# Kernel optimization log

Measured on AMD Instinct MI355X. Metric: run time of the kernel, lower is better.

Reference implementation:

```python
import jax, jax.numpy as jnp
import numpy as np


def setup_inputs() -> dict:
    key = jax.random.key(0)
    ks = jax.random.split(key, 8)
    B, S, D, H = 32, 8192, 256, 256  # batch, seq_len, input_dim, hidden_dim
    bound = 1.0 / np.sqrt(H)
    x = jax.random.normal(ks[0], (B, H), dtype=jnp.float32)
    context = jax.random.normal(ks[1], (B, S, D), dtype=jnp.float32)
    mask = jax.random.randint(ks[2], (B, S), 0, 2, dtype=jnp.int32)
    # input_linear: Linear(H, H)
    W_in = jax.random.uniform(ks[3], (H, H), jnp.float32, -bound, bound)
    b_in = jax.random.uniform(ks[4], (H,), jnp.float32, -bound, bound)
    # context_linear: Conv1d(D, H, kernel=1) == pointwise linear over features
    W_ctx = jax.random.uniform(ks[5], (H, D), jnp.float32, -1.0 / np.sqrt(D), 1.0 / np.sqrt(D))
    b_ctx = jax.random.uniform(ks[6], (H,), jnp.float32, -1.0 / np.sqrt(D), 1.0 / np.sqrt(D))
    V = jax.random.uniform(ks[7], (H,), jnp.float32, -bound, bound)
    return {"x": x, "context": context, "mask": mask,
            "W_in": W_in, "b_in": b_in, "W_ctx": W_ctx, "b_ctx": b_ctx, "V": V}


def reference(x, context, mask, W_in, b_in, W_ctx, b_ctx, V):
    # inp: [B, H] -> broadcast over seq as [B, 1, H]
    inp = (x @ W_in.T + b_in)[:, None, :]
    # ctx: Conv1d(kernel=1) over permuted context == per-position linear: [B, S, H]
    ctx = jnp.einsum('bsd,hd->bsh', context, W_ctx) + b_ctx
    # score: V . tanh(inp + ctx) reduced over H -> [B, S]
    att = jnp.einsum('bsh,h->bs', jnp.tanh(inp + ctx), V)
    att = 10.0 * jnp.tanh(att)
    att = jnp.where(mask.astype(bool), att, -jnp.inf)
    ans = jax.nn.softmax(att, axis=1)
    indices = jnp.argmax(ans, axis=1)
    p = jnp.max(ans, axis=1)
    return (indices, p[:, None], mask.astype(bool))
```

## Files before the change

### kernel.cpp

```cpp
#include <hip/hip_runtime.h>
#include <math.h>

#define S_LEN 8192
#define BATCH 32
#define HDIM 256
#define DDIM 256
#define TS 32
#define LDK 264

typedef float f32x4 __attribute__((ext_vector_type(4)));
typedef __fp16 h16x2 __attribute__((ext_vector_type(2)));
typedef __fp16 h16x4 __attribute__((ext_vector_type(4)));
typedef _Float16 f16x4 __attribute__((ext_vector_type(4)));
typedef _Float16 f16x8 __attribute__((ext_vector_type(8)));

static __device__ __forceinline__ float fast_tanh(float x) {
    float e = __expf(2.0f * x);
    return 1.0f - 2.0f / (e + 1.0f);
}

__global__ void prep_kernel(const float* __restrict__ x,
                            const float* __restrict__ W_in,
                            const float* __restrict__ b_in,
                            const float* __restrict__ W_ctx,
                            const float* __restrict__ b_ctx,
                            float* __restrict__ cin,
                            _Float16* __restrict__ Wf) {
    __shared__ float xs[DDIM];
    const int bx = blockIdx.x;
    const int t  = threadIdx.x;
    if (bx < BATCH) {
        xs[t] = x[bx * DDIM + t];
        __syncthreads();
        const float* wr = W_in + t * DDIM;
        float acc = b_in[t] + b_ctx[t];
        #pragma unroll 8
        for (int d = 0; d < DDIM; ++d) acc += xs[d] * wr[d];
        cin[bx * HDIM + t] = acc;
    } else {
        const int g  = (bx - BATCH) * 256 + t;
        const int nt = g >> 9;
        const int ks = (g >> 6) & 7;
        const int l  = g & 63;
        const int h  = nt * 16 + (l & 15);
        const int d0 = ks * 32 + (l >> 4) * 8;
        const float* src = W_ctx + h * DDIM + d0;
        f16x8 vh;
        #pragma unroll
        for (int j = 0; j < 8; ++j) vh[j] = (_Float16)src[j];
        *(f16x8*)(Wf + (size_t)g * 8) = vh;
    }
}

__launch_bounds__(256, 4)
__global__ void att_kernel(const float* __restrict__ context,
                           const int* __restrict__ mask,
                           const float* __restrict__ cin,
                           const float* __restrict__ V,
                           const _Float16* __restrict__ Wf,
                           float* __restrict__ att,
                           float* __restrict__ out_mask) {
    __shared__ _Float16 a_hi[TS * LDK];
    __shared__ _Float16 a_lo[TS * LDK];
    __shared__ float cin_s[HDIM];
    __shared__ float v_s[HDIM];
    __shared__ float att_part[4][TS];

    const int sblk = blockIdx.x;
    const int b    = blockIdx.y;
    const int t    = threadIdx.x;
    const int w    = t >> 6;
    const int l    = t & 63;
    const int lane16 = l & 15;
    const int q      = l >> 4;

    cin_s[t] = cin[b * HDIM + t];
    v_s[t]   = V[t];

    const float* cbase = context + ((size_t)b * S_LEN + (size_t)sblk * TS) * DDIM;
    #pragma unroll
    for (int i = 0; i < 8; ++i) {
        int f   = i * 256 + t;
        int row = f >> 6;
        int c4  = f & 63;
        f32x4 v = *(const f32x4*)(cbase + row * DDIM + c4 * 4);
        h16x2 h0 = __builtin_amdgcn_cvt_pkrtz(v[0], v[1]);
        h16x2 h1 = __builtin_amdgcn_cvt_pkrtz(v[2], v[3]);
        h16x2 l0 = __builtin_amdgcn_cvt_pkrtz(v[0] - (float)h0[0], v[1] - (float)h0[1]);
        h16x2 l1 = __builtin_amdgcn_cvt_pkrtz(v[2] - (float)h1[0], v[3] - (float)h1[1]);
        h16x4 hi; hi[0] = h0[0]; hi[1] = h0[1]; hi[2] = h1[0]; hi[3] = h1[1];
        h16x4 lo; lo[0] = l0[0]; lo[1] = l0[1]; lo[2] = l1[0]; lo[3] = l1[1];
        *(h16x4*)(a_hi + row * LDK + c4 * 4) = hi;
        *(h16x4*)(a_lo + row * LDK + c4 * 4) = lo;
    }
    __syncthreads();

    f32x4 acc[2][4];
    #pragma unroll
    for (int mt = 0; mt < 2; ++mt)
        #pragma unroll
        for (int i = 0; i < 4; ++i) acc[mt][i] = (f32x4){0.f, 0.f, 0.f, 0.f};

    const int ntb = w * 4;
    #pragma unroll
    for (int ks = 0; ks < 8; ++ks) {
        f16x8 bh[4];
        #pragma unroll
        for (int i = 0; i < 4; ++i) {
            int off = (((ntb + i) * 8 + ks) * 64 + l) * 8;
            bh[i] = *(const f16x8*)(Wf + off);
        }
        f16x8 ah[2], al[2];
        #pragma unroll
        for (int mt = 0; mt < 2; ++mt) {
            int o = (mt * 16 + lane16) * LDK + ks * 32 + q * 8;
            ah[mt] = *(const f16x8*)(a_hi + o);
            al[mt] = *(const f16x8*)(a_lo + o);
        }
        #pragma unroll
        for (int mt = 0; mt < 2; ++mt)
            #pragma unroll
            for (int i = 0; i < 4; ++i) {
                acc[mt][i] = __builtin_amdgcn_mfma_f32_16x16x32_f16(ah[mt], bh[i], acc[mt][i], 0, 0, 0);
                acc[mt][i] = __builtin_amdgcn_mfma_f32_16x16x32_f16(al[mt], bh[i], acc[mt][i], 0, 0, 0);
            }
    }

    float part[2][4] = {};
    #pragma unroll
    for (int i = 0; i < 4; ++i) {
        int h = (ntb + i) * 16 + lane16;
        float c  = cin_s[h];
        float vv = v_s[h];
        #pragma unroll
        for (int mt = 0; mt < 2; ++mt)
            #pragma unroll
            for (int r = 0; r < 4; ++r)
                part[mt][r] += fast_tanh(acc[mt][i][r] + c) * vv;
    }
    #pragma unroll
    for (int mt = 0; mt < 2; ++mt)
        #pragma unroll
        for (int r = 0; r < 4; ++r) {
            float v = part[mt][r];
            v += __shfl_xor(v, 1);
            v += __shfl_xor(v, 2);
            v += __shfl_xor(v, 4);
            v += __shfl_xor(v, 8);
            part[mt][r] = v;
        }
    if (lane16 == 0) {
        #pragma unroll
        for (int mt = 0; mt < 2; ++mt)
            #pragma unroll
            for (int r = 0; r < 4; ++r)
                att_part[w][mt * 16 + q * 4 + r] = part[mt][r];
    }
    __syncthreads();

    if (t < TS) {
        float a = att_part[0][t] + att_part[1][t] + att_part[2][t] + att_part[3][t];
        a = 10.0f * fast_tanh(a);
        int s  = sblk * TS + t;
        int mk = mask[b * S_LEN + s];
        att[(size_t)b * S_LEN + s] = mk ? a : -INFINITY;
        out_mask[(size_t)b * S_LEN + s] = mk ? 1.0f : 0.0f;
    }
}

__global__ void reduce_kernel(const float* __restrict__ att,
                              float* __restrict__ out) {
    __shared__ float smax[256];
    __shared__ int   sidx[256];
    const int b = blockIdx.x;
    const int t = threadIdx.x;
    const float* row = att + (size_t)b * S_LEN;

    float best = -INFINITY;
    int   bid  = 0x7fffffff;
    for (int s = t; s < S_LEN; s += 256) {
        float v = row[s];
        if (v > best) { best = v; bid = s; }
    }
    smax[t] = best; sidx[t] = bid;
    __syncthreads();
    for (int off = 128; off > 0; off >>= 1) {
        if (t < off) {
            float ov = smax[t + off]; int oi = sidx[t + off];
            if (ov > smax[t] || (ov == smax[t] && oi < sidx[t])) { smax[t] = ov; sidx[t] = oi; }
        }
        __syncthreads();
    }
    const float mx = smax[0];
    const int   ix = sidx[0];
    __syncthreads();

    float sum = 0.f;
    for (int s = t; s < S_LEN; s += 256)
        sum += __expf(row[s] - mx);
    smax[t] = sum;
    __syncthreads();
    for (int off = 128; off > 0; off >>= 1) {
        if (t < off) smax[t] += smax[t + off];
        __syncthreads();
    }
    if (t == 0) {
        out[b]         = (float)ix;
        out[BATCH + b] = 1.0f / smax[0];
    }
}

extern "C" void kernel_launch(void* const* d_in, const int* in_sizes, int n_in,
                              void* d_out, int out_size, void* d_ws, size_t ws_size,
                              hipStream_t stream) {
    const float* x       = (const float*)d_in[0];
    const float* context = (const float*)d_in[1];
    const int*   mask    = (const int*)d_in[2];
    const float* W_in    = (const float*)d_in[3];
    const float* b_in    = (const float*)d_in[4];
    const float* W_ctx   = (const float*)d_in[5];
    const float* b_ctx   = (const float*)d_in[6];
    const float* V       = (const float*)d_in[7];
    float* out = (float*)d_out;

    char* ws = (char*)d_ws;
    float*    cin = (float*)ws;
    _Float16* Wf  = (_Float16*)(ws + 32 * 1024);
    float*    att = (float*)(ws + 160 * 1024);

    float* out_mask = out + 64;

    prep_kernel<<<64, 256, 0, stream>>>(x, W_in, b_in, W_ctx, b_ctx, cin, Wf);
    dim3 grid(S_LEN / TS, BATCH);
    att_kernel<<<grid, 256, 0, stream>>>(context, mask, cin, V, Wf, att, out_mask);
    reduce_kernel<<<BATCH, 256, 0, stream>>>(att, out);
}
```

Before: 434.6 us.

## Persistent 1024-thread blocks with register-resident W and double-buffered context tiles

Each block now handles 512 sequence positions in 8 sub-tiles of 64, using 16 waves. Each wave keeps its 16-row slice of the fp16 W_ctx in registers and swaps the MFMA operand roles. The next context sub-tile is prefetched into registers and converted into a second LDS buffer while the current one is computed. This removes repeated global W loads per block and overlaps context loads with MFMA work. In exchange the grid is much smaller (512 blocks of 1024 threads), which raises register pressure and lowers occupancy.

```diff
diff --git a/kernel.cpp b/kernel.cpp
--- a/kernel.cpp
+++ b/kernel.cpp
@@ -5,18 +5,30 @@
 #define BATCH 32
 #define HDIM 256
 #define DDIM 256
-#define TS 32
+#define SCHUNK 512
+#define NSUB 8
+#define TSUB 64
 #define LDK 264
 
 typedef float f32x4 __attribute__((ext_vector_type(4)));
 typedef __fp16 h16x2 __attribute__((ext_vector_type(2)));
 typedef __fp16 h16x4 __attribute__((ext_vector_type(4)));
-typedef _Float16 f16x4 __attribute__((ext_vector_type(4)));
 typedef _Float16 f16x8 __attribute__((ext_vector_type(8)));
 
 static __device__ __forceinline__ float fast_tanh(float x) {
     float e = __expf(2.0f * x);
     return 1.0f - 2.0f / (e + 1.0f);
+}
+
+static __device__ __forceinline__ void cvt_store(f32x4 v, _Float16* ph, _Float16* pl) {
+    h16x2 h0 = __builtin_amdgcn_cvt_pkrtz(v[0], v[1]);
+    h16x2 h1 = __builtin_amdgcn_cvt_pkrtz(v[2], v[3]);
+    h16x2 l0 = __builtin_amdgcn_cvt_pkrtz(v[0] - (float)h0[0], v[1] - (float)h0[1]);
+    h16x2 l1 = __builtin_amdgcn_cvt_pkrtz(v[2] - (float)h1[0], v[3] - (float)h1[1]);
+    h16x4 hi; hi[0] = h0[0]; hi[1] = h0[1]; hi[2] = h1[0]; hi[3] = h1[1];
+    h16x4 lo; lo[0] = l0[0]; lo[1] = l0[1]; lo[2] = l1[0]; lo[3] = l1[1];
+    *(h16x4*)ph = hi;
+    *(h16x4*)pl = lo;
 }
 
 __global__ void prep_kernel(const float* __restrict__ x,
@@ -39,10 +51,10 @@
         cin[bx * HDIM + t] = acc;
     } else {
         const int g  = (bx - BATCH) * 256 + t;
-        const int nt = g >> 9;
+        const int ht = g >> 9;
         const int ks = (g >> 6) & 7;
         const int l  = g & 63;
-        const int h  = nt * 16 + (l & 15);
+        const int h  = ht * 16 + (l & 15);
         const int d0 = ks * 32 + (l >> 4) * 8;
         const float* src = W_ctx + h * DDIM + d0;
         f16x8 vh;
@@ -52,7 +64,7 @@
     }
 }
 
-__launch_bounds__(256, 4)
+__launch_bounds__(1024, 4)
 __global__ void att_kernel(const float* __restrict__ context,
                            const int* __restrict__ mask,
                            const float* __restrict__ cin,
@@ -60,111 +72,101 @@
                            const _Float16* __restrict__ Wf,
                            float* __restrict__ att,
                            float* __restrict__ out_mask) {
-    __shared__ _Float16 a_hi[TS * LDK];
-    __shared__ _Float16 a_lo[TS * LDK];
-    __shared__ float cin_s[HDIM];
-    __shared__ float v_s[HDIM];
-    __shared__ float att_part[4][TS];
-
-    const int sblk = blockIdx.x;
-    const int b    = blockIdx.y;
-    const int t    = threadIdx.x;
-    const int w    = t >> 6;
-    const int l    = t & 63;
+    __shared__ __align__(16) _Float16 a_hi[2][TSUB * LDK];
+    __shared__ __align__(16) _Float16 a_lo[2][TSUB * LDK];
+    __shared__ float att_part[2][16][TSUB];
+
+    const int schunk = blockIdx.x;
+    const int b      = blockIdx.y;
+    const int t      = threadIdx.x;
+    const int w      = t >> 6;
+    const int l      = t & 63;
     const int lane16 = l & 15;
     const int q      = l >> 4;
 
-    cin_s[t] = cin[b * HDIM + t];
-    v_s[t]   = V[t];
-
-    const float* cbase = context + ((size_t)b * S_LEN + (size_t)sblk * TS) * DDIM;
+    f16x8 wfrag[8];
     #pragma unroll
-    for (int i = 0; i < 8; ++i) {
-        int f   = i * 256 + t;
-        int row = f >> 6;
-        int c4  = f & 63;
-        f32x4 v = *(const f32x4*)(cbase + row * DDIM + c4 * 4);
-        h16x2 h0 = __builtin_amdgcn_cvt_pkrtz(v[0], v[1]);
-        h16x2 h1 = __builtin_amdgcn_cvt_pkrtz(v[2], v[3]);
-        h16x2 l0 = __builtin_amdgcn_cvt_pkrtz(v[0] - (float)h0[0], v[1] - (float)h0[1]);
-        h16x2 l1 = __builtin_amdgcn_cvt_pkrtz(v[2] - (float)h1[0], v[3] - (float)h1[1]);
-        h16x4 hi; hi[0] = h0[0]; hi[1] = h0[1]; hi[2] = h1[0]; hi[3] = h1[1];
-        h16x4 lo; lo[0] = l0[0]; lo[1] = l0[1]; lo[2] = l1[0]; lo[3] = l1[1];
-        *(h16x4*)(a_hi + row * LDK + c4 * 4) = hi;
-        *(h16x4*)(a_lo + row * LDK + c4 * 4) = lo;
-    }
-    __syncthreads();
-
-    f32x4 acc[2][4];
+    for (int ks = 0; ks < 8; ++ks)
+        wfrag[ks] = *(const f16x8*)(Wf + (size_t)((w * 8 + ks) * 64 + l) * 8);
+
+    float cinr[4], vr[4];
     #pragma unroll
-    for (int mt = 0; mt < 2; ++mt)
-        #pragma unroll
-        for (int i = 0; i < 4; ++i) acc[mt][i] = (f32x4){0.f, 0.f, 0.f, 0.f};
-
-    const int ntb = w * 4;
-    #pragma unroll
-    for (int ks = 0; ks < 8; ++ks) {
-        f16x8 bh[4];
-        #pragma unroll
-        for (int i = 0; i < 4; ++i) {
-            int off = (((ntb + i) * 8 + ks) * 64 + l) * 8;
-            bh[i] = *(const f16x8*)(Wf + off);
-        }
-        f16x8 ah[2], al[2];
-        #pragma unroll
-        for (int mt = 0; mt < 2; ++mt) {
-            int o = (mt * 16 + lane16) * LDK + ks * 32 + q * 8;
-            ah[mt] = *(const f16x8*)(a_hi + o);
-            al[mt] = *(const f16x8*)(a_lo + o);
-        }
-        #pragma unroll
-        for (int mt = 0; mt < 2; ++mt)
-            #pragma unroll
-            for (int i = 0; i < 4; ++i) {
-                acc[mt][i] = __builtin_amdgcn_mfma_f32_16x16x32_f16(ah[mt], bh[i], acc[mt][i], 0, 0, 0);
-                acc[mt][i] = __builtin_amdgcn_mfma_f32_16x16x32_f16(al[mt], bh[i], acc[mt][i], 0, 0, 0);
-            }
-    }
-
-    float part[2][4] = {};
+    for (int r = 0; r < 4; ++r) {
+        int h = w * 16 + q * 4 + r;
+        cinr[r] = cin[b * HDIM + h];
+        vr[r]   = V[h];
+    }
+
+    const float* cbase = context + ((size_t)b * S_LEN + (size_t)schunk * SCHUNK) * DDIM;
+
     #pragma unroll
     for (int i = 0; i < 4; ++i) {
-        int h = (ntb + i) * 16 + lane16;
-        float c  = cin_s[h];
-        float vv = v_s[h];
-        #pragma unroll
-        for (int mt = 0; mt < 2; ++mt)
+        int f = i * 1024 + t, row = f >> 6, c4 = f & 63;
+        f32x4 v = *(const f32x4*)(cbase + row * DDIM + c4 * 4);
+        cvt_store(v, &a_hi[0][row * LDK + c4 * 4], &a_lo[0][row * LDK + c4 * 4]);
+    }
+    __syncthreads();
+
+    for (int it = 0; it < NSUB; ++it) {
+        const int cur = it & 1;
+        const bool pre = (it + 1 < NSUB);
+
+        f32x4 pf[4];
+        if (pre) {
+            const float* nb = cbase + (size_t)(it + 1) * TSUB * DDIM;
+            #pragma unroll
+            for (int i = 0; i < 4; ++i) {
+                int f = i * 1024 + t, row = f >> 6, c4 = f & 63;
+                pf[i] = *(const f32x4*)(nb + row * DDIM + c4 * 4);
+            }
+        }
+
+        f32x4 acc[4];
+        #pragma unroll
+        for (int nt = 0; nt < 4; ++nt) acc[nt] = (f32x4){0.f, 0.f, 0.f, 0.f};
+        #pragma unroll
+        for (int ks = 0; ks < 8; ++ks) {
+            #pragma unroll
+            for (int nt = 0; nt < 4; ++nt) {
+                int o = (nt * 16 + lane16) * LDK + ks * 32 + q * 8;
+                f16x8 bh = *(const f16x8*)(&a_hi[cur][o]);
+                f16x8 bl = *(const f16x8*)(&a_lo[cur][o]);
+                acc[nt] = __builtin_amdgcn_mfma_f32_16x16x32_f16(wfrag[ks], bh, acc[nt], 0, 0, 0);
+                acc[nt] = __builtin_amdgcn_mfma_f32_16x16x32_f16(wfrag[ks], bl, acc[nt], 0, 0, 0);
+            }
+        }
+
+        #pragma unroll
+        for (int nt = 0; nt < 4; ++nt) {
+            float p = 0.f;
             #pragma unroll
             for (int r = 0; r < 4; ++r)
-                part[mt][r] += fast_tanh(acc[mt][i][r] + c) * vv;
-    }
-    #pragma unroll
-    for (int mt = 0; mt < 2; ++mt)
-        #pragma unroll
-        for (int r = 0; r < 4; ++r) {
-            float v = part[mt][r];
-            v += __shfl_xor(v, 1);
-            v += __shfl_xor(v, 2);
-            v += __shfl_xor(v, 4);
-            v += __shfl_xor(v, 8);
-            part[mt][r] = v;
-        }
-    if (lane16 == 0) {
-        #pragma unroll
-        for (int mt = 0; mt < 2; ++mt)
-            #pragma unroll
-            for (int r = 0; r < 4; ++r)
-                att_part[w][mt * 16 + q * 4 + r] = part[mt][r];
-    }
-    __syncthreads();
-
-    if (t < TS) {
-        float a = att_part[0][t] + att_part[1][t] + att_part[2][t] + att_part[3][t];
-        a = 10.0f * fast_tanh(a);
-        int s  = sblk * TS + t;
-        int mk = mask[b * S_LEN + s];
-        att[(size_t)b * S_LEN + s] = mk ? a : -INFINITY;
-        out_mask[(size_t)b * S_LEN + s] = mk ? 1.0f : 0.0f;
+                p += fast_tanh(acc[nt][r] + cinr[r]) * vr[r];
+            p += __shfl_xor(p, 16);
+            p += __shfl_xor(p, 32);
+            if (l < 16) att_part[cur][w][nt * 16 + l] = p;
+        }
+
+        if (pre) {
+            #pragma unroll
+            for (int i = 0; i < 4; ++i) {
+                int f = i * 1024 + t, row = f >> 6, c4 = f & 63;
+                cvt_store(pf[i], &a_hi[cur ^ 1][row * LDK + c4 * 4],
+                                 &a_lo[cur ^ 1][row * LDK + c4 * 4]);
+            }
+        }
+        __syncthreads();
+
+        if (t < TSUB) {
+            float a = 0.f;
+            #pragma unroll
+            for (int ww = 0; ww < 16; ++ww) a += att_part[cur][ww][t];
+            a = 10.0f * fast_tanh(a);
+            int s  = schunk * SCHUNK + it * TSUB + t;
+            int mk = mask[b * S_LEN + s];
+            att[(size_t)b * S_LEN + s]      = mk ? a : -INFINITY;
+            out_mask[(size_t)b * S_LEN + s] = mk ? 1.0f : 0.0f;
+        }
     }
 }
 
@@ -231,7 +233,7 @@
     float* out_mask = out + 64;
 
     prep_kernel<<<64, 256, 0, stream>>>(x, W_in, b_in, W_ctx, b_ctx, cin, Wf);
-    dim3 grid(S_LEN / TS, BATCH);
-    att_kernel<<<grid, 256, 0, stream>>>(context, mask, cin, V, Wf, att, out_mask);
+    dim3 grid(S_LEN / SCHUNK, BATCH);
+    att_kernel<<<grid, 1024, 0, stream>>>(context, mask, cin, V, Wf, att, out_mask);
     reduce_kernel<<<BATCH, 256, 0, stream>>>(att, out);
 }
```

Result: faster. 418.3 us (-3.7%).
